# Optimization experiments

Hardware: AMD Instinct MI355X
Metric: run time of the kernel (lower is better)

The kernel has to match this reference:

```python
import jax, jax.numpy as jnp
import numpy as np

EPS = 1e-08
SURROGATE_SCALE = 10.0  # SuperSpike surrogate slope

@jax.custom_vjp
def spike_fn(v):
    # Heaviside forward, SuperSpike surrogate gradient backward
    return (v > 0).astype(v.dtype)

def _spike_fwd(v):
    return spike_fn(v), v

def _spike_bwd(v, g):
    return (g / (1.0 + SURROGATE_SCALE * jnp.abs(v)) ** 2,)

spike_fn.defvjp(_spike_fwd, _spike_bwd)


def setup_inputs() -> dict:
    key = jax.random.key(0)
    k1, k2, k3, k4 = jax.random.split(key, 4)
    B, C, T = 64, 256, 2048
    x = jax.random.normal(k1, (B, C, T), dtype=jnp.float32)
    conv_weight = jax.random.normal(k2, (C, C, 3), dtype=jnp.float32) * 0.05
    beta = jnp.clip(0.7 + 0.01 * jax.random.normal(k3, (1,), dtype=jnp.float32), 0.0, 1.0)
    b = jnp.clip(1.0 + 0.01 * jax.random.normal(k4, (C,), dtype=jnp.float32), 0.0, None)
    return {"x": x, "conv_weight": conv_weight, "beta": beta, "b": b}


def reference(x, conv_weight, beta, b):
    # x: (B, C, T); LIF recurrence over T with scaled threshold/reset
    norm = (conv_weight ** 2).sum((1, 2))          # (C,)
    inv_norm = 1.0 / (norm + EPS)                   # (C,)
    B, C, T = x.shape
    xt = jnp.transpose(x, (2, 0, 1))                # (T, B, C)

    def step(carry, inp):
        mem, spk = carry
        rst = spk * (b * norm)                      # einsum ab,b,b->ab
        mem = (mem - rst) * beta + inp * (1.0 - beta)
        mthr = mem * inv_norm - b
        spk = spike_fn(mthr)
        return (mem, spk), spk

    init = (jnp.zeros((B, C), x.dtype), jnp.zeros((B, C), x.dtype))
    _, spk_rec = jax.lax.scan(step, init, xt)       # (T, B, C)
    return jnp.transpose(spk_rec, (1, 2, 0))        # (B, C, T), flatten_output=False
```

## Files before the change

kernel.cpp:

```cpp
#include <hip/hip_runtime.h>

#define C_DIM 256
#define T_DIM 2048
#define B_DIM 64
#define NROWS (B_DIM * C_DIM)
#define RPB 64
#define TW 256
#define NT (T_DIM / TW)
#define RSTRIDE 260

__device__ __forceinline__ float sqrn(float v) { return __fmul_rn(v, v); }

__global__ __launch_bounds__(64) void norm_kernel(const float* __restrict__ w,
                                                  const float* __restrict__ b,
                                                  float* __restrict__ bn,
                                                  float* __restrict__ ninv) {
    const int c = blockIdx.x;
    const int k = threadIdx.x;
    __shared__ float q[8];
    if (k < 8) {
        const float* a = w + c * 768 + k * 96;
        float r0 = sqrn(a[0]), r1 = sqrn(a[1]), r2 = sqrn(a[2]), r3 = sqrn(a[3]);
        float r4 = sqrn(a[4]), r5 = sqrn(a[5]), r6 = sqrn(a[6]), r7 = sqrn(a[7]);
        #pragma unroll
        for (int i = 8; i < 96; i += 8) {
            r0 = __fadd_rn(r0, sqrn(a[i + 0]));
            r1 = __fadd_rn(r1, sqrn(a[i + 1]));
            r2 = __fadd_rn(r2, sqrn(a[i + 2]));
            r3 = __fadd_rn(r3, sqrn(a[i + 3]));
            r4 = __fadd_rn(r4, sqrn(a[i + 4]));
            r5 = __fadd_rn(r5, sqrn(a[i + 5]));
            r6 = __fadd_rn(r6, sqrn(a[i + 6]));
            r7 = __fadd_rn(r7, sqrn(a[i + 7]));
        }
        q[k] = __fadd_rn(__fadd_rn(__fadd_rn(r0, r1), __fadd_rn(r2, r3)),
                         __fadd_rn(__fadd_rn(r4, r5), __fadd_rn(r6, r7)));
    }
    __syncthreads();
    if (k == 0) {
        float s = __fadd_rn(__fadd_rn(__fadd_rn(q[0], q[1]), __fadd_rn(q[2], q[3])),
                            __fadd_rn(__fadd_rn(q[4], q[5]), __fadd_rn(q[6], q[7])));
        bn[c]   = __fmul_rn(b[c], s);
        ninv[c] = 1.0f / __fadd_rn(s, 1e-8f);
    }
}

__device__ __forceinline__ float lif_step(float xv, float& mem, float& spk,
                                          float bnc, float beta, float omb,
                                          float nic, float bc) {
    float rst  = __fmul_rn(spk, bnc);
    mem        = __fadd_rn(__fmul_rn(__fsub_rn(mem, rst), beta),
                           __fmul_rn(xv, omb));
    float mthr = __fsub_rn(__fmul_rn(mem, nic), bc);
    spk        = (mthr > 0.0f) ? 1.0f : 0.0f;
    return spk;
}

#define WAITCNT_VM0    0x0F70
#define WAITCNT_VM62   0xCF7E
#define WAITCNT_LGKM0  0xC07F

#define LDS_PTR(p) ((__attribute__((address_space(3))) void*)(p))
#define GLB_PTR(p) ((const __attribute__((address_space(1))) void*)(p))

__global__ __launch_bounds__(64, 1) void lif_kernel(const float* __restrict__ x,
                                                    const float* __restrict__ beta_p,
                                                    const float* __restrict__ b,
                                                    const float* __restrict__ bn,
                                                    const float* __restrict__ ninv,
                                                    float* __restrict__ out) {
    __shared__ __align__(16) float lds[2][RPB * RSTRIDE];

    const int lane = threadIdx.x;
    const int row0 = blockIdx.x * RPB;
    const int c    = (row0 + lane) & (C_DIM - 1);

    const float beta = beta_p[0];
    const float omb  = __fsub_rn(1.0f, beta);
    const float bnc  = bn[c];
    const float nic  = ninv[c];
    const float bc   = b[c];

    const float* xbase = x + (size_t)row0 * T_DIM + lane * 4;
    float*       obase = out + (size_t)row0 * T_DIM + lane * 4;

    #pragma unroll
    for (int r = 0; r < RPB; ++r) {
        __builtin_amdgcn_global_load_lds(GLB_PTR(xbase + (size_t)r * T_DIM),
                                         LDS_PTR(&lds[0][r * RSTRIDE]), 16, 0, 0);
    }

    float mem = 0.0f, spk = 0.0f;

    #pragma unroll 1
    for (int k = 0; k < NT; ++k) {
        if (k == 0) __builtin_amdgcn_s_waitcnt(WAITCNT_VM0);
        else        __builtin_amdgcn_s_waitcnt(WAITCNT_VM62);

        if (k + 1 < NT) {
            const float* xt = xbase + (size_t)(k + 1) * TW;
            #pragma unroll
            for (int r = 0; r < RPB; ++r) {
                __builtin_amdgcn_global_load_lds(GLB_PTR(xt + (size_t)r * T_DIM),
                                                 LDS_PTR(&lds[(k + 1) & 1][r * RSTRIDE]),
                                                 16, 0, 0);
            }
        }

        float* buf = &lds[k & 1][0];
        float* myrow = buf + lane * RSTRIDE;
        #pragma unroll 4
        for (int g = 0; g < TW / 4; ++g) {
            float4 v = *(const float4*)(myrow + 4 * g);
            float4 o;
            o.x = lif_step(v.x, mem, spk, bnc, beta, omb, nic, bc);
            o.y = lif_step(v.y, mem, spk, bnc, beta, omb, nic, bc);
            o.z = lif_step(v.z, mem, spk, bnc, beta, omb, nic, bc);
            o.w = lif_step(v.w, mem, spk, bnc, beta, omb, nic, bc);
            *(float4*)(myrow + 4 * g) = o;
        }

        __builtin_amdgcn_s_waitcnt(WAITCNT_LGKM0);

        float* ot = obase + (size_t)k * TW;
        #pragma unroll
        for (int r = 0; r < RPB; ++r) {
            float4 v = *(const float4*)(buf + r * RSTRIDE + 4 * lane);
            *(float4*)(ot + (size_t)r * T_DIM) = v;
        }
    }
}

extern "C" void kernel_launch(void* const* d_in, const int* in_sizes, int n_in,
                              void* d_out, int out_size, void* d_ws, size_t ws_size,
                              hipStream_t stream) {
    const float* x    = (const float*)d_in[0];
    const float* w    = (const float*)d_in[1];
    const float* beta = (const float*)d_in[2];
    const float* b    = (const float*)d_in[3];
    float* out  = (float*)d_out;
    float* bn   = (float*)d_ws;
    float* ninv = bn + C_DIM;

    norm_kernel<<<C_DIM, 64, 0, stream>>>(w, b, bn, ninv);
    lif_kernel<<<NROWS / RPB, 64, 0, stream>>>(x, beta, b, bn, ninv, out);
}
```

Measured before the change: 284.8 us.

## Process two rows per thread with interleaved recurrences and shorter dependency chain

Each thread now advances two independent LIF rows in lockstep, doubling rows per block and halving time-tile width, so LDS usage stays similar. Spike state is kept as a boolean and the threshold compare is done directly against b, removing a subtract from the serial chain. This adds instruction-level parallelism to hide ALU latency, but halves the number of blocks to 128, which leaves many CUs idle and doubles memory traffic per wave.

```diff
diff --git a/kernel.cpp b/kernel.cpp
--- a/kernel.cpp
+++ b/kernel.cpp
@@ -4,10 +4,11 @@
 #define T_DIM 2048
 #define B_DIM 64
 #define NROWS (B_DIM * C_DIM)
-#define RPB 64
-#define TW 256
-#define NT (T_DIM / TW)
-#define RSTRIDE 260
+#define RPB   128
+#define PAIRS 64
+#define TW    128
+#define NT    (T_DIM / TW)
+#define GSTR  260
 
 __device__ __forceinline__ float sqrn(float v) { return __fmul_rn(v, v); }
 
@@ -45,15 +46,19 @@
     }
 }
 
-__device__ __forceinline__ float lif_step(float xv, float& mem, float& spk,
-                                          float bnc, float beta, float omb,
-                                          float nic, float bc) {
-    float rst  = __fmul_rn(spk, bnc);
-    mem        = __fadd_rn(__fmul_rn(__fsub_rn(mem, rst), beta),
-                           __fmul_rn(xv, omb));
-    float mthr = __fsub_rn(__fmul_rn(mem, nic), bc);
-    spk        = (mthr > 0.0f) ? 1.0f : 0.0f;
-    return spk;
+__device__ __forceinline__ void step2(float xa, float xb_,
+                                      float& memA, float& memB, bool& sA, bool& sB,
+                                      float& oa, float& ob_,
+                                      float bnA, float bnB, float beta, float omb,
+                                      float niA, float niB, float bcA, float bcB) {
+    float rA = sA ? bnA : 0.0f;
+    float rB = sB ? bnB : 0.0f;
+    memA = __fadd_rn(__fmul_rn(__fsub_rn(memA, rA), beta), __fmul_rn(xa,  omb));
+    memB = __fadd_rn(__fmul_rn(__fsub_rn(memB, rB), beta), __fmul_rn(xb_, omb));
+    sA = __fmul_rn(memA, niA) > bcA;
+    sB = __fmul_rn(memB, niB) > bcB;
+    oa  = sA ? 1.0f : 0.0f;
+    ob_ = sB ? 1.0f : 0.0f;
 }
 
 #define WAITCNT_VM0    0x0F70
@@ -69,28 +74,31 @@
                                                     const float* __restrict__ bn,
                                                     const float* __restrict__ ninv,
                                                     float* __restrict__ out) {
-    __shared__ __align__(16) float lds[2][RPB * RSTRIDE];
+    __shared__ __align__(16) float lds[2][PAIRS * GSTR];
 
     const int lane = threadIdx.x;
     const int row0 = blockIdx.x * RPB;
-    const int c    = (row0 + lane) & (C_DIM - 1);
+    const int rowA = row0 + 2 * lane;
+    const int cA = rowA & (C_DIM - 1);
+    const int cB = (rowA + 1) & (C_DIM - 1);
 
     const float beta = beta_p[0];
     const float omb  = __fsub_rn(1.0f, beta);
-    const float bnc  = bn[c];
-    const float nic  = ninv[c];
-    const float bc   = b[c];
+    const float bnA = bn[cA], bnB = bn[cB];
+    const float niA = ninv[cA], niB = ninv[cB];
+    const float bcA = b[cA],   bcB = b[cB];
 
-    const float* xbase = x + (size_t)row0 * T_DIM + lane * 4;
-    float*       obase = out + (size_t)row0 * T_DIM + lane * 4;
+    const size_t lrow = (size_t)(lane >> 5) * T_DIM + (size_t)(lane & 31) * 4;
+    const float* xb = x   + (size_t)row0 * T_DIM + lrow;
+    float*       ob = out + (size_t)row0 * T_DIM + lrow;
 
     #pragma unroll
-    for (int r = 0; r < RPB; ++r) {
-        __builtin_amdgcn_global_load_lds(GLB_PTR(xbase + (size_t)r * T_DIM),
-                                         LDS_PTR(&lds[0][r * RSTRIDE]), 16, 0, 0);
-    }
+    for (int r = 0; r < PAIRS; ++r)
+        __builtin_amdgcn_global_load_lds(GLB_PTR(xb + (size_t)(2 * r) * T_DIM),
+                                         LDS_PTR(&lds[0][r * GSTR]), 16, 0, 0);
 
-    float mem = 0.0f, spk = 0.0f;
+    float memA = 0.0f, memB = 0.0f;
+    bool  sA = false, sB = false;
 
     #pragma unroll 1
     for (int k = 0; k < NT; ++k) {
@@ -98,35 +106,37 @@
         else        __builtin_amdgcn_s_waitcnt(WAITCNT_VM62);
 
         if (k + 1 < NT) {
-            const float* xt = xbase + (size_t)(k + 1) * TW;
+            const float* xt = xb + (size_t)(k + 1) * TW;
             #pragma unroll
-            for (int r = 0; r < RPB; ++r) {
-                __builtin_amdgcn_global_load_lds(GLB_PTR(xt + (size_t)r * T_DIM),
-                                                 LDS_PTR(&lds[(k + 1) & 1][r * RSTRIDE]),
+            for (int r = 0; r < PAIRS; ++r)
+                __builtin_amdgcn_global_load_lds(GLB_PTR(xt + (size_t)(2 * r) * T_DIM),
+                                                 LDS_PTR(&lds[(k + 1) & 1][r * GSTR]),
                                                  16, 0, 0);
-            }
         }
 
         float* buf = &lds[k & 1][0];
-        float* myrow = buf + lane * RSTRIDE;
+        float* mA  = buf + lane * GSTR;
+        float* mB  = mA + TW;
         #pragma unroll 4
         for (int g = 0; g < TW / 4; ++g) {
-            float4 v = *(const float4*)(myrow + 4 * g);
-            float4 o;
-            o.x = lif_step(v.x, mem, spk, bnc, beta, omb, nic, bc);
-            o.y = lif_step(v.y, mem, spk, bnc, beta, omb, nic, bc);
-            o.z = lif_step(v.z, mem, spk, bnc, beta, omb, nic, bc);
-            o.w = lif_step(v.w, mem, spk, bnc, beta, omb, nic, bc);
-            *(float4*)(myrow + 4 * g) = o;
+            float4 va = *(const float4*)(mA + 4 * g);
+            float4 vb = *(const float4*)(mB + 4 * g);
+            float4 oa, obv;
+            step2(va.x, vb.x, memA, memB, sA, sB, oa.x, obv.x, bnA, bnB, beta, omb, niA, niB, bcA, bcB);
+            step2(va.y, vb.y, memA, memB, sA, sB, oa.y, obv.y, bnA, bnB, beta, omb, niA, niB, bcA, bcB);
+            step2(va.z, vb.z, memA, memB, sA, sB, oa.z, obv.z, bnA, bnB, beta, omb, niA, niB, bcA, bcB);
+            step2(va.w, vb.w, memA, memB, sA, sB, oa.w, obv.w, bnA, bnB, beta, omb, niA, niB, bcA, bcB);
+            *(float4*)(mA + 4 * g) = oa;
+            *(float4*)(mB + 4 * g) = obv;
         }
 
         __builtin_amdgcn_s_waitcnt(WAITCNT_LGKM0);
 
-        float* ot = obase + (size_t)k * TW;
+        float* ot = ob + (size_t)k * TW;
         #pragma unroll
-        for (int r = 0; r < RPB; ++r) {
-            float4 v = *(const float4*)(buf + r * RSTRIDE + 4 * lane);
-            *(float4*)(ot + (size_t)r * T_DIM) = v;
+        for (int r = 0; r < PAIRS; ++r) {
+            float4 v = *(const float4*)(buf + r * GSTR + 4 * lane);
+            *(float4*)(ot + (size_t)(2 * r) * T_DIM) = v;
         }
     }
 }
```

Measured after the change: 332.4 us. 1.17x slower.
